# Kernel tuning notes

Measured on AMD Instinct MI355X. Metric: run time of the kernel, lower is better.

## Reference

```python
import jax, jax.numpy as jnp
import numpy as np

B, T_TEXT, D, T_TOTAL = 16, 1024, 512, 2048


def setup_inputs() -> dict:
    key = jax.random.key(0)
    k1, k2 = jax.random.split(key)
    enc = jax.random.normal(k1, (B, T_TEXT, D), dtype=jnp.float32)
    dur = jax.random.uniform(k2, (B, T_TEXT), dtype=jnp.float32, minval=0.5, maxval=1.5)
    # rescale so each batch's total duration is exactly T_TOTAL -> round(sum)=T_TOTAL,
    # making T_mel = T_TOTAL + 1 (torch.range(0, max) is inclusive) a static shape.
    dur = dur * (T_TOTAL / jnp.sum(dur, axis=-1, keepdims=True))
    return {"encoder_outputs": enc, "duration": dur, "t_mel": T_TOTAL + 1}


def reference(encoder_outputs, duration, t_mel):
    # encoder_outputs: [B, T_text, D]; duration: [B, T_text]; t_mel: static int
    t_tot = jnp.round(jnp.sum(duration, axis=-1, keepdims=True))      # [B, 1]
    e = jnp.cumsum(duration, axis=-1)                                  # [B, T_text]
    c = e - 0.5 * t_tot                                                # [B, T_text]
    t = jnp.arange(t_mel, dtype=duration.dtype)                        # [T_mel]
    # Gaussian kernel logits over (frame time - center) distances
    logits = -0.1 * (t[None, None, :] - c[:, :, None]) ** 2            # [B, T_text, T_mel]
    # exp / sum-over-text == softmax over axis=1 (numerically stable form)
    w = jax.nn.softmax(logits, axis=1)                                 # [B, T_text, T_mel]
    # w^T @ encoder_outputs  ->  [B, T_mel, D]
    return jnp.einsum('btm,btd->bmd', w, encoder_outputs)
```

## Files before the change

### kernel.cpp

```cpp
#include <hip/hip_runtime.h>
#include <math.h>

#define B_   16
#define TT   1024
#define D_   512
#define TMEL 2049
#define TM   16
#define KB   64
#define NTILE ((TMEL + TM - 1) / TM)

typedef float nfloat4 __attribute__((ext_vector_type(4)));

__global__ __launch_bounds__(256) void expand_fused(const float* __restrict__ enc,
                                                    const float* __restrict__ dur,
                                                    float* __restrict__ out) {
    const int b    = blockIdx.y;
    const int tile = blockIdx.x;
    const int m0   = tile * TM;
    const int t    = threadIdx.x;
    const int lane = t & 63;
    const int wid  = t >> 6;

    __shared__ float s_c[TT];
    __shared__ float s_wsum[4];
    __shared__ float s_red[256];
    __shared__ float s_fmax[TM], s_finv[TM];
    __shared__ float s_w[KB * TM];

    float4 v = ((const float4*)(dur + (size_t)b * TT))[t];
    float l0 = v.x;
    float l1 = l0 + v.y;
    float l2 = l1 + v.z;
    float l3 = l2 + v.w;
    float x = l3;
    #pragma unroll
    for (int off = 1; off < 64; off <<= 1) {
        float y = __shfl_up(x, off);
        if (lane >= off) x += y;
    }
    if (lane == 63) s_wsum[wid] = x;
    __syncthreads();
    float w0 = s_wsum[0], w1 = s_wsum[1], w2 = s_wsum[2], w3 = s_wsum[3];
    float tot  = w0 + w1 + w2 + w3;
    float wpre = (wid > 0 ? w0 : 0.f) + (wid > 1 ? w1 : 0.f) + (wid > 2 ? w2 : 0.f);
    float excl = wpre + (x - l3);
    float h = 0.5f * roundf(tot);
    s_c[4*t+0] = excl + l0 - h;
    s_c[4*t+1] = excl + l1 - h;
    s_c[4*t+2] = excl + l2 - h;
    s_c[4*t+3] = excl + l3 - h;
    __syncthreads();

    const int m1c = min(m0 + TM - 1, TMEL - 1);
    const float lo = (float)m0 - 16.f;
    const float hi = (float)m1c + 16.f;
    int a, z, mid;
    a = 0; z = TT; while (a < z) { mid = (a + z) >> 1; if (s_c[mid] <  lo) a = mid + 1; else z = mid; } const int j0  = a;
    a = 0; z = TT; while (a < z) { mid = (a + z) >> 1; if (s_c[mid] <= hi) a = mid + 1; else z = mid; } const int j1  = a;
    a = 0; z = TT; while (a < z) { mid = (a + z) >> 1; if (s_c[mid] < (float)m0)  a = mid + 1; else z = mid; } const int jc0 = a;
    a = 0; z = TT; while (a < z) { mid = (a + z) >> 1; if (s_c[mid] < (float)m1c) a = mid + 1; else z = mid; } const int jc1 = a;
    int ilo = min(j0, jc0 - 8);  if (ilo < 0)  ilo = 0;
    int ihi = max(j1, jc1 + 9);  if (ihi > TT) ihi = TT;

    const int f  = t & 15;
    const int sl = t >> 4;
    const int mmf = min(m0 + f, TMEL - 1);
    const float fm = (float)mmf;
    float lmax = -3.4e38f;
    for (int i = ilo + sl; i < ihi; i += 16) {
        float d = fm - s_c[i];
        lmax = fmaxf(lmax, -0.1f * d * d);
    }
    s_red[t] = lmax;
    __syncthreads();
    #pragma unroll
    for (int st = 128; st >= 16; st >>= 1) {
        if (t < st) s_red[t] = fmaxf(s_red[t], s_red[t + st]);
        __syncthreads();
    }
    if (t < TM) s_fmax[t] = s_red[t];
    __syncthreads();
    const float myfmax = s_fmax[f];
    float lsum = 0.f;
    for (int i = ilo + sl; i < ihi; i += 16) {
        float d = fm - s_c[i];
        lsum += __expf(-0.1f * d * d - myfmax);
    }
    s_red[t] = lsum;
    __syncthreads();
    #pragma unroll
    for (int st = 128; st >= 16; st >>= 1) {
        if (t < st) s_red[t] += s_red[t + st];
        __syncthreads();
    }
    if (t < TM) s_finv[t] = 1.f / s_red[t];
    __syncthreads();

    const int fg = t >> 7;
    const int dt = t & 127;
    const int d0 = dt * 4;
    const int frbase = fg * 8;
    float4 acc[8];
    #pragma unroll
    for (int j = 0; j < 8; ++j) acc[j] = make_float4(0.f, 0.f, 0.f, 0.f);
    const float* encb = enc + (size_t)b * TT * D_;

    for (int k0 = ilo; k0 < ihi; k0 += KB) {
        const int kn = min(KB, ihi - k0);
        __syncthreads();
        for (int p = t; p < kn * TM; p += 256) {
            const int il = p >> 4;
            const int fr = p & 15;
            const int mf = min(m0 + fr, TMEL - 1);
            float d = (float)mf - s_c[k0 + il];
            s_w[p] = __expf(-0.1f * d * d - s_fmax[fr]) * s_finv[fr];
        }
        __syncthreads();
        for (int il = 0; il < kn; ++il) {
            const float4 ev = *(const float4*)(encb + (size_t)(k0 + il) * D_ + d0);
            const float4 wa = *(const float4*)(s_w + il * TM + frbase);
            const float4 wb = *(const float4*)(s_w + il * TM + frbase + 4);
            acc[0].x += wa.x * ev.x; acc[0].y += wa.x * ev.y; acc[0].z += wa.x * ev.z; acc[0].w += wa.x * ev.w;
            acc[1].x += wa.y * ev.x; acc[1].y += wa.y * ev.y; acc[1].z += wa.y * ev.z; acc[1].w += wa.y * ev.w;
            acc[2].x += wa.z * ev.x; acc[2].y += wa.z * ev.y; acc[2].z += wa.z * ev.z; acc[2].w += wa.z * ev.w;
            acc[3].x += wa.w * ev.x; acc[3].y += wa.w * ev.y; acc[3].z += wa.w * ev.z; acc[3].w += wa.w * ev.w;
            acc[4].x += wb.x * ev.x; acc[4].y += wb.x * ev.y; acc[4].z += wb.x * ev.z; acc[4].w += wb.x * ev.w;
            acc[5].x += wb.y * ev.x; acc[5].y += wb.y * ev.y; acc[5].z += wb.y * ev.z; acc[5].w += wb.y * ev.w;
            acc[6].x += wb.z * ev.x; acc[6].y += wb.z * ev.y; acc[6].z += wb.z * ev.z; acc[6].w += wb.z * ev.w;
            acc[7].x += wb.w * ev.x; acc[7].y += wb.w * ev.y; acc[7].z += wb.w * ev.z; acc[7].w += wb.w * ev.w;
        }
    }

    #pragma unroll
    for (int j = 0; j < 8; ++j) {
        const int mm2 = m0 + frbase + j;
        if (mm2 < TMEL) {
            nfloat4* dst = (nfloat4*)(out + ((size_t)b * TMEL + mm2) * D_ + d0);
            nfloat4 av = { acc[j].x, acc[j].y, acc[j].z, acc[j].w };
            __builtin_nontemporal_store(av, dst);
        }
    }
}

extern "C" void kernel_launch(void* const* d_in, const int* in_sizes, int n_in,
                              void* d_out, int out_size, void* d_ws, size_t ws_size,
                              hipStream_t stream) {
    const float* enc = (const float*)d_in[0];
    const float* dur = (const float*)d_in[1];
    float* out = (float*)d_out;
    (void)d_ws; (void)ws_size;

    dim3 grid(NTILE, B_);
    expand_fused<<<grid, 256, 0, stream>>>(enc, dur, out);
}
```

Before: 104.7 us.

## Replace binary searches and shared-memory reductions with wavefront shuffles

The four serial binary searches over the centres array are replaced by per-thread checks on the thread's own four centres, followed by wavefront min/max shuffles and a four-entry shared combine. Each wavefront now owns four frames, so the per-frame max and sum reductions use xor shuffles instead of barrier-heavy shared-memory tree reductions. The barrier at the top of the weight-tile loop moves to the end and is skipped after the last tile. This removes many barriers and serial LDS latency from the prologue, which matters because each block's main loop is short. The range detection assumes the centres are sorted, as the old searches did.

```diff
diff --git a/kernel.cpp b/kernel.cpp
--- a/kernel.cpp
+++ b/kernel.cpp
@@ -23,7 +23,7 @@
 
     __shared__ float s_c[TT];
     __shared__ float s_wsum[4];
-    __shared__ float s_red[256];
+    __shared__ int4  s_ij[4];
     __shared__ float s_fmax[TM], s_finv[TM];
     __shared__ float s_w[KB * TM];
 
@@ -45,25 +45,45 @@
     float wpre = (wid > 0 ? w0 : 0.f) + (wid > 1 ? w1 : 0.f) + (wid > 2 ? w2 : 0.f);
     float excl = wpre + (x - l3);
     float h = 0.5f * roundf(tot);
-    s_c[4*t+0] = excl + l0 - h;
-    s_c[4*t+1] = excl + l1 - h;
-    s_c[4*t+2] = excl + l2 - h;
-    s_c[4*t+3] = excl + l3 - h;
+    const float c0 = excl + l0 - h;
+    const float c1 = excl + l1 - h;
+    const float c2 = excl + l2 - h;
+    const float c3 = excl + l3 - h;
+    s_c[4*t+0] = c0;
+    s_c[4*t+1] = c1;
+    s_c[4*t+2] = c2;
+    s_c[4*t+3] = c3;
+
+    const int   m1c = min(m0 + TM - 1, TMEL - 1);
+    const float lo  = (float)m0 - 16.f;
+    const float hi  = (float)m1c + 16.f;
+    const float fm0 = (float)m0;
+    const float fm1 = (float)m1c;
+    const int base = 4 * t;
+    int j0  = (c0 >= lo)  ? base : (c1 >= lo)  ? base+1 : (c2 >= lo)  ? base+2 : (c3 >= lo)  ? base+3 : TT;
+    int j1  = (c3 <= hi)  ? base+3 : (c2 <= hi) ? base+2 : (c1 <= hi) ? base+1 : (c0 <= hi) ? base : -1;
+    int jc0 = (c0 >= fm0) ? base : (c1 >= fm0) ? base+1 : (c2 >= fm0) ? base+2 : (c3 >= fm0) ? base+3 : TT;
+    int jc1 = (c0 >= fm1) ? base : (c1 >= fm1) ? base+1 : (c2 >= fm1) ? base+2 : (c3 >= fm1) ? base+3 : TT;
+    #pragma unroll
+    for (int off = 32; off; off >>= 1) {
+        j0  = min(j0,  __shfl_xor(j0,  off));
+        j1  = max(j1,  __shfl_xor(j1,  off));
+        jc0 = min(jc0, __shfl_xor(jc0, off));
+        jc1 = min(jc1, __shfl_xor(jc1, off));
+    }
+    if (lane == 0) s_ij[wid] = make_int4(j0, j1, jc0, jc1);
     __syncthreads();
+    int4 r0 = s_ij[0], r1 = s_ij[1], r2 = s_ij[2], r3 = s_ij[3];
+    const int J0  = min(min(r0.x, r1.x), min(r2.x, r3.x));
+    const int J1  = max(max(r0.y, r1.y), max(r2.y, r3.y)) + 1;
+    const int JC0 = min(min(r0.z, r1.z), min(r2.z, r3.z));
+    const int JC1 = min(min(r0.w, r1.w), min(r2.w, r3.w));
+    int ilo = min(J0, JC0 - 8);  if (ilo < 0)  ilo = 0;
+    int ihi = max(J1, JC1 + 9);  if (ihi > TT) ihi = TT;
 
-    const int m1c = min(m0 + TM - 1, TMEL - 1);
-    const float lo = (float)m0 - 16.f;
-    const float hi = (float)m1c + 16.f;
-    int a, z, mid;
-    a = 0; z = TT; while (a < z) { mid = (a + z) >> 1; if (s_c[mid] <  lo) a = mid + 1; else z = mid; } const int j0  = a;
-    a = 0; z = TT; while (a < z) { mid = (a + z) >> 1; if (s_c[mid] <= hi) a = mid + 1; else z = mid; } const int j1  = a;
-    a = 0; z = TT; while (a < z) { mid = (a + z) >> 1; if (s_c[mid] < (float)m0)  a = mid + 1; else z = mid; } const int jc0 = a;
-    a = 0; z = TT; while (a < z) { mid = (a + z) >> 1; if (s_c[mid] < (float)m1c) a = mid + 1; else z = mid; } const int jc1 = a;
-    int ilo = min(j0, jc0 - 8);  if (ilo < 0)  ilo = 0;
-    int ihi = max(j1, jc1 + 9);  if (ihi > TT) ihi = TT;
-
-    const int f  = t & 15;
-    const int sl = t >> 4;
+    const int fiw = lane & 3;
+    const int sl  = lane >> 2;
+    const int f   = (wid << 2) | fiw;
     const int mmf = min(m0 + f, TMEL - 1);
     const float fm = (float)mmf;
     float lmax = -3.4e38f;
@@ -71,29 +91,19 @@
         float d = fm - s_c[i];
         lmax = fmaxf(lmax, -0.1f * d * d);
     }
-    s_red[t] = lmax;
-    __syncthreads();
     #pragma unroll
-    for (int st = 128; st >= 16; st >>= 1) {
-        if (t < st) s_red[t] = fmaxf(s_red[t], s_red[t + st]);
-        __syncthreads();
-    }
-    if (t < TM) s_fmax[t] = s_red[t];
-    __syncthreads();
-    const float myfmax = s_fmax[f];
+    for (int off = 4; off < 64; off <<= 1) lmax = fmaxf(lmax, __shfl_xor(lmax, off));
     float lsum = 0.f;
     for (int i = ilo + sl; i < ihi; i += 16) {
         float d = fm - s_c[i];
-        lsum += __expf(-0.1f * d * d - myfmax);
+        lsum += __expf(-0.1f * d * d - lmax);
     }
-    s_red[t] = lsum;
-    __syncthreads();
     #pragma unroll
-    for (int st = 128; st >= 16; st >>= 1) {
-        if (t < st) s_red[t] += s_red[t + st];
-        __syncthreads();
+    for (int off = 4; off < 64; off <<= 1) lsum += __shfl_xor(lsum, off);
+    if (lane < 4) {
+        s_fmax[(wid << 2) | lane] = lmax;
+        s_finv[(wid << 2) | lane] = 1.f / lsum;
     }
-    if (t < TM) s_finv[t] = 1.f / s_red[t];
     __syncthreads();
 
     const int fg = t >> 7;
@@ -107,7 +117,6 @@
 
     for (int k0 = ilo; k0 < ihi; k0 += KB) {
         const int kn = min(KB, ihi - k0);
-        __syncthreads();
         for (int p = t; p < kn * TM; p += 256) {
             const int il = p >> 4;
             const int fr = p & 15;
@@ -129,6 +138,7 @@
             acc[6].x += wb.z * ev.x; acc[6].y += wb.z * ev.y; acc[6].z += wb.z * ev.z; acc[6].w += wb.z * ev.w;
             acc[7].x += wb.w * ev.x; acc[7].y += wb.w * ev.y; acc[7].z += wb.w * ev.z; acc[7].w += wb.w * ev.w;
         }
+        if (k0 + KB < ihi) __syncthreads();
     }
 
     #pragma unroll
```

Measured after the change: 102.9 us. Within noise of the previous version (-1.7%).
